# Optimization experiments

Hardware: AMD Instinct MI355X
Metric: run time of the kernel (lower is better)

The kernel has to match this reference:

```python
import jax, jax.numpy as jnp
import numpy as np

EPS = 0.1  # global `eps` in original repo (width scale)


def _parts(x, c, w):
    # x: (N,3), c: (N1,3), w: (N1,3)
    x1 = x[:, 0:1] - c[:, 0]  # (N, N1)
    y1 = x[:, 1:2] - c[:, 1]
    z1 = x[:, 2:3] - c[:, 2]
    d = w * w  # (N1, 3)
    e = jnp.exp(-(x1 * x1 * d[:, 0] + y1 * y1 * d[:, 1] + z1 * z1 * d[:, 2]))
    return x1, y1, z1, d, e


def _u(e, h):
    return e @ h  # (N,)


def _du(diff, dcoef, e, h):
    return ((-2.0 * diff * dcoef) * e) @ h  # (N,)


def setup_inputs() -> dict:
    key = jax.random.key(0)
    ks = jax.random.split(key, 13)
    N, N1 = 32768, 1024
    x = jax.random.uniform(ks[0], (N, 3), dtype=jnp.float32)
    def params(k1, k2, k3):
        h = jax.random.uniform(k1, (N1,), dtype=jnp.float32)
        c = jax.random.uniform(k2, (N1, 3), dtype=jnp.float32)
        w = 5.0 * jax.random.uniform(k3, (N1, 3), dtype=jnp.float32) / EPS
        return h, c, w
    h1, c1, w1 = params(ks[1], ks[2], ks[3])
    h2, c2, w2 = params(ks[4], ks[5], ks[6])
    h3, c3, w3 = params(ks[7], ks[8], ks[9])
    h4, c4, w4 = params(ks[10], ks[11], ks[12])
    return {"x": x, "h1": h1, "c1": c1, "w1": w1,
            "h2": h2, "c2": c2, "w2": w2,
            "h3": h3, "c3": c3, "w3": w3,
            "h4": h4, "c4": c4, "w4": w4}


def reference(x, h1, c1, w1, h2, c2, w2, h3, c3, w3, h4, c4, w4):
    # Set 1: ux, uy, uz (kernel exp computed once, reused for all 3 derivs)
    x1, y1, z1, d, e = _parts(x, c1, w1)
    ux = _du(x1, d[:, 0], e, h1)
    uy = _du(y1, d[:, 1], e, h1)
    uz = _du(z1, d[:, 2], e, h1)
    # Set 2: P, Px
    x1, y1, z1, d, e = _parts(x, c2, w2)
    P = _u(e, h2)
    Px = _du(x1, d[:, 0], e, h2)
    # Set 3: Q, Qy
    x1, y1, z1, d, e = _parts(x, c3, w3)
    Q = _u(e, h3)
    Qy = _du(y1, d[:, 1], e, h3)
    # Set 4: R, Rz
    x1, y1, z1, d, e = _parts(x, c4, w4)
    R = _u(e, h4)
    Rz = _du(z1, d[:, 2], e, h4)
    return (ux, uy, uz, P, Px, Q, Qy, R, Rz)
```

## Files before the change

### kernel.cpp

```cpp
#include <hip/hip_runtime.h>

typedef float v2f __attribute__((ext_vector_type(2)));

static constexpr float SQRT_LOG2E = 1.2011224087864498f;
static constexpr float NEG_2LN2   = -1.3862943611198906f;

__device__ __forceinline__ v2f sp(float s) { return (v2f){s, s}; }
__device__ __forceinline__ v2f vfma(v2f a, v2f b, v2f c) {
    return __builtin_elementwise_fma(a, b, c);
}

template <int SET>
__device__ __forceinline__ void srbf_body(
    const float* __restrict__ x, const float* __restrict__ h,
    const float* __restrict__ c, const float* __restrict__ w,
    float* __restrict__ dst, int N, int jbase, int jcount, float4* lds)
{
    constexpr int REC = (SET == 0) ? 3 : 2;
    constexpr int OB  = (SET == 0) ? 0 : (2 * SET + 1);
    const int tid = threadIdx.x;

    for (int jj = tid; jj < jcount; jj += 256) {
        const int gj = jbase + jj;
        float hj  = h[gj];
        float w0  = w[3 * gj + 0] * SQRT_LOG2E;
        float w1  = w[3 * gj + 1] * SQRT_LOG2E;
        float w2  = w[3 * gj + 2] * SQRT_LOG2E;
        float cw0 = -c[3 * gj + 0] * w0;
        float cw1 = -c[3 * gj + 1] * w1;
        float cw2 = -c[3 * gj + 2] * w2;
        if constexpr (SET == 0) {
            lds[jj * 3 + 0] = make_float4(w0, w1, w2, cw0);
            lds[jj * 3 + 1] = make_float4(cw1, cw2, NEG_2LN2 * hj * w0, NEG_2LN2 * hj * w1);
            lds[jj * 3 + 2] = make_float4(NEG_2LN2 * hj * w2, 0.f, 0.f, 0.f);
        } else {
            constexpr int K = SET - 1;
            float wk = (K == 0) ? w0 : (K == 1 ? w1 : w2);
            lds[jj * 2 + 0] = make_float4(w0, w1, w2, cw0);
            lds[jj * 2 + 1] = make_float4(cw1, cw2, hj, NEG_2LN2 * hj * wk);
        }
    }
    __syncthreads();

    const int i0 = blockIdx.x * 1024 + tid;
    v2f px[2], py[2], pz[2];
#pragma unroll
    for (int g = 0; g < 2; ++g) {
        const int ia = i0 + 512 * g, ib = ia + 256;
        px[g] = (v2f){x[3 * ia + 0], x[3 * ib + 0]};
        py[g] = (v2f){x[3 * ia + 1], x[3 * ib + 1]};
        pz[g] = (v2f){x[3 * ia + 2], x[3 * ib + 2]};
    }

    v2f a0[2] = {sp(0.f), sp(0.f)};
    v2f a1[2] = {sp(0.f), sp(0.f)};
    v2f a2[2] = {sp(0.f), sp(0.f)};

#pragma unroll 2
    for (int jj = 0; jj < jcount; ++jj) {
        const float4 A = lds[jj * REC + 0];
        const float4 B = lds[jj * REC + 1];
        float b2c = 0.f;
        if constexpr (SET == 0) b2c = lds[jj * 3 + 2].x;
#pragma unroll
        for (int g = 0; g < 2; ++g) {
            v2f t0 = vfma(px[g], sp(A.x), sp(A.w));
            v2f t1 = vfma(py[g], sp(A.y), sp(B.x));
            v2f t2 = vfma(pz[g], sp(A.z), sp(B.y));
            v2f s  = vfma(t0, t0, vfma(t1, t1, t2 * t2));
            v2f e  = (v2f){__builtin_amdgcn_exp2f(-s.x),
                           __builtin_amdgcn_exp2f(-s.y)};
            if constexpr (SET == 0) {
                a0[g] = vfma(t0, sp(B.z) * e, a0[g]);
                a1[g] = vfma(t1, sp(B.w) * e, a1[g]);
                a2[g] = vfma(t2, sp(b2c) * e, a2[g]);
            } else {
                constexpr int K = SET - 1;
                v2f tk = (K == 0) ? t0 : (K == 1 ? t1 : t2);
                a0[g] = vfma(sp(B.z), e, a0[g]);
                a1[g] = vfma(tk, sp(B.w) * e, a1[g]);
            }
        }
    }

#pragma unroll
    for (int g = 0; g < 2; ++g) {
        const int ia = i0 + 512 * g, ib = ia + 256;
        dst[(OB + 0) * N + ia] = a0[g].x;  dst[(OB + 0) * N + ib] = a0[g].y;
        dst[(OB + 1) * N + ia] = a1[g].x;  dst[(OB + 1) * N + ib] = a1[g].y;
        if constexpr (SET == 0) {
            dst[2 * N + ia] = a2[g].x;     dst[2 * N + ib] = a2[g].y;
        }
    }
}

__global__ __launch_bounds__(256) void srbf_kernel(
    const float* x,
    const float* h1, const float* c1, const float* w1,
    const float* h2, const float* c2, const float* w2,
    const float* h3, const float* c3, const float* w3,
    const float* h4, const float* c4, const float* w4,
    float* out, float* ws, int N, int jcount, int split)
{
    extern __shared__ float4 lds[];
    const int jbase = blockIdx.y * jcount;
    float* dst = split ? (ws + (size_t)blockIdx.y * 9 * N) : out;
    switch (blockIdx.z) {
    case 0: srbf_body<0>(x, h1, c1, w1, dst, N, jbase, jcount, lds); break;
    case 1: srbf_body<1>(x, h2, c2, w2, dst, N, jbase, jcount, lds); break;
    case 2: srbf_body<2>(x, h3, c3, w3, dst, N, jbase, jcount, lds); break;
    case 3: srbf_body<3>(x, h4, c4, w4, dst, N, jbase, jcount, lds); break;
    }
}

__global__ __launch_bounds__(256) void reduce_kernel(
    const float* __restrict__ ws, float* __restrict__ out, int total)
{
    const int i = blockIdx.x * 256 + threadIdx.x;
    if (i < total)
        out[i] = (ws[i] + ws[total + i]) + (ws[2 * total + i] + ws[3 * total + i]);
}

extern "C" void kernel_launch(void* const* d_in, const int* in_sizes, int n_in,
                              void* d_out, int out_size, void* d_ws, size_t ws_size,
                              hipStream_t stream)
{
    const float* x = (const float*)d_in[0];
    const int N  = in_sizes[0] / 3;
    const int N1 = in_sizes[1];

    const size_t partial_bytes = (size_t)4 * 9 * N * sizeof(float);
    const bool split = ws_size >= partial_bytes;
    const int JC = split ? 4 : 1;
    const int jcount = N1 / JC;

    dim3 grid(N / 1024, JC, 4);
    const size_t lds_bytes = (size_t)jcount * 3 * sizeof(float4);
    srbf_kernel<<<grid, 256, lds_bytes, stream>>>(
        x,
        (const float*)d_in[1],  (const float*)d_in[2],  (const float*)d_in[3],
        (const float*)d_in[4],  (const float*)d_in[5],  (const float*)d_in[6],
        (const float*)d_in[7],  (const float*)d_in[8],  (const float*)d_in[9],
        (const float*)d_in[10], (const float*)d_in[11], (const float*)d_in[12],
        (float*)d_out, (float*)d_ws, N, jcount, split ? 1 : 0);

    if (split) {
        const int total = 9 * N;
        reduce_kernel<<<(total + 255) / 256, 256, 0, stream>>>(
            (const float*)d_ws, (float*)d_out, total);
    }
}
```

Measured before the change: 42.40 us.

## Increase neuron-dimension split to eight and vectorise generic partial-sum reduction

Splits the center dimension into up to eight chunks, chosen by workspace size, instead of four, doubling the number of blocks for better occupancy on the compute-bound exp loop. The reduce kernel becomes generic over the split count and uses float4 loads and stores. The inner loop unroll goes from 2 to 4. In exchange, more partial buffers are written and read, which adds memory traffic in the reduction pass.

New measurement: 39.17 us. -7.6%, faster.

```diff
diff --git a/kernel.cpp b/kernel.cpp
--- a/kernel.cpp
+++ b/kernel.cpp
@@ -56,7 +56,7 @@
     v2f a1[2] = {sp(0.f), sp(0.f)};
     v2f a2[2] = {sp(0.f), sp(0.f)};
 
-#pragma unroll 2
+#pragma unroll 4
     for (int jj = 0; jj < jcount; ++jj) {
         const float4 A = lds[jj * REC + 0];
         const float4 B = lds[jj * REC + 1];
@@ -104,7 +104,7 @@
 {
     extern __shared__ float4 lds[];
     const int jbase = blockIdx.y * jcount;
-    float* dst = split ? (ws + (size_t)blockIdx.y * 9 * N) : out;
+    float* dst = (split > 1) ? (ws + (size_t)blockIdx.y * 9 * N) : out;
     switch (blockIdx.z) {
     case 0: srbf_body<0>(x, h1, c1, w1, dst, N, jbase, jcount, lds); break;
     case 1: srbf_body<1>(x, h2, c2, w2, dst, N, jbase, jcount, lds); break;
@@ -114,11 +114,19 @@
 }
 
 __global__ __launch_bounds__(256) void reduce_kernel(
-    const float* __restrict__ ws, float* __restrict__ out, int total)
+    const float4* __restrict__ ws, float4* __restrict__ out,
+    int total4, int split)
 {
     const int i = blockIdx.x * 256 + threadIdx.x;
-    if (i < total)
-        out[i] = (ws[i] + ws[total + i]) + (ws[2 * total + i] + ws[3 * total + i]);
+    if (i < total4) {
+        float4 acc = ws[i];
+#pragma unroll 8
+        for (int p = 1; p < split; ++p) {
+            const float4 v = ws[(size_t)p * total4 + i];
+            acc.x += v.x; acc.y += v.y; acc.z += v.z; acc.w += v.w;
+        }
+        out[i] = acc;
+    }
 }
 
 extern "C" void kernel_launch(void* const* d_in, const int* in_sizes, int n_in,
@@ -129,12 +137,15 @@
     const int N  = in_sizes[0] / 3;
     const int N1 = in_sizes[1];
 
-    const size_t partial_bytes = (size_t)4 * 9 * N * sizeof(float);
-    const bool split = ws_size >= partial_bytes;
-    const int JC = split ? 4 : 1;
-    const int jcount = N1 / JC;
+    int split = 1;
+    for (int s = 8; s >= 2; s >>= 1) {
+        if (ws_size >= (size_t)s * 9 * N * sizeof(float) && (N1 % s) == 0) {
+            split = s; break;
+        }
+    }
+    const int jcount = N1 / split;
 
-    dim3 grid(N / 1024, JC, 4);
+    dim3 grid(N / 1024, split, 4);
     const size_t lds_bytes = (size_t)jcount * 3 * sizeof(float4);
     srbf_kernel<<<grid, 256, lds_bytes, stream>>>(
         x,
@@ -142,11 +153,11 @@
         (const float*)d_in[4],  (const float*)d_in[5],  (const float*)d_in[6],
         (const float*)d_in[7],  (const float*)d_in[8],  (const float*)d_in[9],
         (const float*)d_in[10], (const float*)d_in[11], (const float*)d_in[12],
-        (float*)d_out, (float*)d_ws, N, jcount, split ? 1 : 0);
+        (float*)d_out, (float*)d_ws, N, jcount, split);
 
-    if (split) {
-        const int total = 9 * N;
-        reduce_kernel<<<(total + 255) / 256, 256, 0, stream>>>(
-            (const float*)d_ws, (float*)d_out, total);
+    if (split > 1) {
+        const int total4 = 9 * N / 4;
+        reduce_kernel<<<(total4 + 255) / 256, 256, 0, stream>>>(
+            (const float4*)d_ws, (float4*)d_out, total4, split);
     }
 }
```
